# Kernel optimization log

Measured on AMD Instinct MI355X. Metric: run time of the kernel, lower is better.

Reference implementation:

```python
import jax, jax.numpy as jnp
import numpy as np

TABLE_NUM = 16
TABLE_SIZE_LOG2 = 12
T = 1 << TABLE_SIZE_LOG2          # 4096 entries per table
FEAT = 2                          # features per entry (mini_linear in = table_num*2)
Z_DIM = 512
RES_MIN = 16
RES_MAX = 256
IMG = 256
MLP_HIDDEN = 64
OUT_DIM = 3
BATCH = 8
PRIME_Y = np.uint32(2654435761)   # instant-NGP spatial hash prime


def setup_inputs() -> dict:
    key = jax.random.key(0)
    ks = jax.random.split(key, 9)
    d_tab = TABLE_NUM * T * FEAT
    return {
        "z": jax.random.normal(ks[0], (BATCH, Z_DIM), jnp.float32),
        "w_table": jax.random.normal(ks[1], (Z_DIM, d_tab), jnp.float32) * 1e-2,
        "b_table": jnp.zeros((d_tab,), jnp.float32),
        "w1": jax.random.normal(ks[2], (TABLE_NUM * FEAT, MLP_HIDDEN), jnp.float32) * (1.0 / np.sqrt(TABLE_NUM * FEAT)),
        "b1": jnp.zeros((MLP_HIDDEN,), jnp.float32),
        "w2": jax.random.normal(ks[3], (MLP_HIDDEN, MLP_HIDDEN), jnp.float32) * (1.0 / np.sqrt(MLP_HIDDEN)),
        "b2": jnp.zeros((MLP_HIDDEN,), jnp.float32),
        "w3": jax.random.normal(ks[4], (MLP_HIDDEN, OUT_DIM), jnp.float32) * (1.0 / np.sqrt(MLP_HIDDEN)),
        "b3": jnp.zeros((OUT_DIM,), jnp.float32),
    }


def _sample_coords(b):
    c = (jnp.arange(IMG, dtype=jnp.float32) + 0.5) / IMG
    xx, yy = jnp.meshgrid(c, c, indexing="ij")  # torch.meshgrid default
    coords = jnp.stack([xx, yy], axis=-1).reshape(1, -1, 2)
    return jnp.broadcast_to(coords, (b, IMG * IMG, 2))


def _hash_retrieve(tables, coords):
    """tables: B x L x T x F; coords: B x N x 2 in [0,1). Returns B x N x (L*F)."""
    B, L, _, _ = tables.shape
    growth = np.exp((np.log(RES_MAX) - np.log(RES_MIN)) / (L - 1))
    offs = jnp.array([[0, 0], [1, 0], [0, 1], [1, 1]], dtype=jnp.uint32)  # 4 corners
    bidx = jnp.arange(B)[:, None, None]
    feats = []
    for l in range(L):
        res = jnp.float32(RES_MIN * (growth ** l))
        pos = coords * res                      # B,N,2
        pos0 = jnp.floor(pos)
        frac = pos - pos0                       # B,N,2
        corner = pos0.astype(jnp.uint32)[:, :, None, :] + offs[None, None]  # B,N,4,2
        idx = (corner[..., 0] ^ (corner[..., 1] * PRIME_Y)) & jnp.uint32(T - 1)
        f = tables[:, l][bidx, idx.astype(jnp.int32)]        # B,N,4,F gather
        fx, fy = frac[..., 0], frac[..., 1]
        w = jnp.stack([(1 - fx) * (1 - fy), fx * (1 - fy),
                       (1 - fx) * fy,       fx * fy], axis=-1)  # B,N,4
        feats.append(jnp.einsum("bncf,bnc->bnf", f, w))
    return jnp.concatenate(feats, axis=-1)


def reference(z, w_table, b_table, w1, b1, w2, b2, w3, b3):
    B = z.shape[0]
    tables = (z @ w_table + b_table).reshape(B, TABLE_NUM, T, FEAT)
    coords = _sample_coords(B).astype(tables.dtype)
    feat = _hash_retrieve(tables, coords)                    # B,N,L*F
    h = jax.nn.relu(feat @ w1 + b1)
    h = jax.nn.relu(h @ w2 + b2)
    o = jnp.tanh(h @ w3 + b3)                                # B,N,3
    return o.reshape(B, IMG, IMG, OUT_DIM).transpose(0, 3, 1, 2)
```

## Files before the change

kernel.cpp:

```cpp
#include <hip/hip_runtime.h>
#include <cmath>

#define TABLE_NUM 16
#define T_SIZE    4096
#define Z_DIM     512
#define IMG       256
#define D_TAB     (TABLE_NUM * T_SIZE * 2)
#define BATCH     8
#define HID       64
#define N_PIX     (IMG * IMG)
#define PRIME_Y   2654435761u
#define KCHUNK    4
#define KLEN      (Z_DIM / KCHUNK)
#define NG4       (D_TAB / 4)

typedef _Float16 v8h  __attribute__((ext_vector_type(8)));
typedef _Float16 v2h  __attribute__((ext_vector_type(2)));
typedef float    v4f  __attribute__((ext_vector_type(4)));

struct ResArr { float r[TABLE_NUM]; };

__global__ void prep_weights(const float* __restrict__ w1, const float* __restrict__ w2,
                             const float* __restrict__ w3, const float* __restrict__ z,
                             _Float16* __restrict__ w1T, _Float16* __restrict__ w2T,
                             _Float16* __restrict__ w3T, float* __restrict__ zT)
{
    const int t = threadIdx.x;
    for (int i = t; i < HID * 32; i += 256) {
        int n = i >> 5, k = i & 31;
        w1T[i] = (_Float16)w1[k * HID + n];
    }
    for (int i = t; i < HID * HID; i += 256) {
        int n = i >> 6, k = i & 63;
        w2T[i] = (_Float16)w2[k * HID + n];
    }
    for (int i = t; i < 16 * HID; i += 256) {
        int n = i >> 6, k = i & 63;
        w3T[i] = (_Float16)(n < 3 ? w3[k * 3 + n] : 0.f);
    }
    for (int i = t; i < Z_DIM * BATCH; i += 256) {
        int k = i >> 3, b = i & 7;
        zT[i] = z[b * Z_DIM + k];
    }
}

__global__ __launch_bounds__(256) void gen_partial(
    const float* __restrict__ zT, const float* __restrict__ w,
    float* __restrict__ part)
{
    const int c  = blockIdx.x >> 7;
    const int g  = (blockIdx.x & 127) * 256 + threadIdx.x;
    const int k0 = c * KLEN;
    const float4* wp = reinterpret_cast<const float4*>(w) + g;

    float4 acc[BATCH];
#pragma unroll
    for (int b = 0; b < BATCH; ++b) acc[b] = make_float4(0.f, 0.f, 0.f, 0.f);

#pragma unroll 8
    for (int kk = 0; kk < KLEN; ++kk) {
        const int k = k0 + kk;
        float4 wv = wp[(size_t)k * NG4];
        const float* zr = zT + k * BATCH;
#pragma unroll
        for (int b = 0; b < BATCH; ++b) {
            float zv = zr[b];
            acc[b].x = fmaf(zv, wv.x, acc[b].x);
            acc[b].y = fmaf(zv, wv.y, acc[b].y);
            acc[b].z = fmaf(zv, wv.z, acc[b].z);
            acc[b].w = fmaf(zv, wv.w, acc[b].w);
        }
    }

    float4* pp = reinterpret_cast<float4*>(part);
#pragma unroll
    for (int b = 0; b < BATCH; ++b)
        pp[((size_t)(c * BATCH + b) << 15) + g] = acc[b];
}

__global__ __launch_bounds__(256) void gen_reduce(
    const float* __restrict__ part, const float* __restrict__ bt,
    float* __restrict__ tabs)
{
    const int i = blockIdx.x * 256 + threadIdx.x;
    const int b = i >> 15, g = i & (NG4 - 1);
    const float4* pp = reinterpret_cast<const float4*>(part);

    float4 s = pp[((size_t)b << 15) + g];
#pragma unroll
    for (int c = 1; c < KCHUNK; ++c) {
        float4 p = pp[((size_t)(c * BATCH + b) << 15) + g];
        s.x += p.x; s.y += p.y; s.z += p.z; s.w += p.w;
    }
    float4 bv = reinterpret_cast<const float4*>(bt)[g];
    s.x += bv.x; s.y += bv.y; s.z += bv.z; s.w += bv.w;
    reinterpret_cast<float4*>(tabs)[((size_t)b << 15) + g] = s;
}

__global__ __launch_bounds__(256) void hash_mlp(
    const float* __restrict__ tabs,
    const _Float16* __restrict__ w1T, const _Float16* __restrict__ w2T,
    const _Float16* __restrict__ w3T,
    const float* __restrict__ b1, const float* __restrict__ b2,
    const float* __restrict__ b3,
    float* __restrict__ out, ResArr res)
{
    __shared__ _Float16 mbuf[4][64][72];
    const int tid  = threadIdx.x;
    const int wid  = tid >> 6;
    const int lane = tid & 63;
    const int b    = blockIdx.x & 7;
    const int tile = blockIdx.x >> 3;
    const int i0   = (tile >> 4) * 16 + wid * 4;
    const int j0   = (tile & 15) * 16;

    const int di = lane >> 4, dj = lane & 15;
    const float cx = ((float)(i0 + di) + 0.5f) * (1.0f / IMG);
    const float cy = ((float)(j0 + dj) + 0.5f) * (1.0f / IMG);
    const float2* tb2 = reinterpret_cast<const float2*>(tabs + (size_t)b * D_TAB);

#pragma unroll 4
    for (int l = 0; l < TABLE_NUM; ++l) {
        float r  = res.r[l];
        float px = cx * r, py = cy * r;
        float fx0 = floorf(px), fy0 = floorf(py);
        float fx = px - fx0, fy = py - fy0;
        unsigned x0 = (unsigned)(int)fx0, y0 = (unsigned)(int)fy0;
        unsigned hy0 = y0 * PRIME_Y, hy1 = (y0 + 1u) * PRIME_Y;
        unsigned i00 = (x0 ^ hy0) & (T_SIZE - 1);
        unsigned i10 = ((x0 + 1u) ^ hy0) & (T_SIZE - 1);
        unsigned i01 = (x0 ^ hy1) & (T_SIZE - 1);
        unsigned i11 = ((x0 + 1u) ^ hy1) & (T_SIZE - 1);
        const float2* tl = tb2 + l * T_SIZE;
        float2 f00 = tl[i00], f10 = tl[i10], f01 = tl[i01], f11 = tl[i11];
        float w00 = (1.f - fx) * (1.f - fy);
        float w10 = fx * (1.f - fy);
        float w01 = (1.f - fx) * fy;
        float w11 = fx * fy;
        float e0 = f00.x * w00 + f10.x * w10 + f01.x * w01 + f11.x * w11;
        float e1 = f00.y * w00 + f10.y * w10 + f01.y * w01 + f11.y * w11;
        v2h p; p.x = (_Float16)e0; p.y = (_Float16)e1;
        *reinterpret_cast<v2h*>(&mbuf[wid][lane][2 * l]) = p;
    }

    const int arow = lane & 15;
    const int kgrp = lane >> 4;

    float bias1v[4], bias2v[4];
#pragma unroll
    for (int nt = 0; nt < 4; ++nt) {
        bias1v[nt] = b1[nt * 16 + arow];
        bias2v[nt] = b2[nt * 16 + arow];
    }
    const float bias3 = (arow < 3) ? b3[arow] : 0.f;

    v8h a1[4];
#pragma unroll
    for (int mt = 0; mt < 4; ++mt)
        a1[mt] = *reinterpret_cast<const v8h*>(&mbuf[wid][mt * 16 + arow][kgrp * 8]);

    v4f c1[4][4];
#pragma unroll
    for (int nt = 0; nt < 4; ++nt) {
        v8h bf1 = *reinterpret_cast<const v8h*>(&w1T[(nt * 16 + arow) * 32 + kgrp * 8]);
#pragma unroll
        for (int mt = 0; mt < 4; ++mt) {
            v4f c = {0.f, 0.f, 0.f, 0.f};
            c = __builtin_amdgcn_mfma_f32_16x16x32_f16(a1[mt], bf1, c, 0, 0, 0);
#pragma unroll
            for (int e = 0; e < 4; ++e)
                c1[mt][nt][e] = fmaxf(c[e] + bias1v[nt], 0.f);
        }
    }

#pragma unroll
    for (int mt = 0; mt < 4; ++mt)
#pragma unroll
        for (int nt = 0; nt < 4; ++nt)
#pragma unroll
            for (int e = 0; e < 4; ++e)
                mbuf[wid][mt * 16 + kgrp * 4 + e][nt * 16 + arow] = (_Float16)c1[mt][nt][e];

    v8h a2[4][2];
#pragma unroll
    for (int mt = 0; mt < 4; ++mt) {
        a2[mt][0] = *reinterpret_cast<const v8h*>(&mbuf[wid][mt * 16 + arow][kgrp * 8]);
        a2[mt][1] = *reinterpret_cast<const v8h*>(&mbuf[wid][mt * 16 + arow][32 + kgrp * 8]);
    }
    v4f c2[4][4];
#pragma unroll
    for (int nt = 0; nt < 4; ++nt) {
        v8h bf2a = *reinterpret_cast<const v8h*>(&w2T[(nt * 16 + arow) * 64 + kgrp * 8]);
        v8h bf2b = *reinterpret_cast<const v8h*>(&w2T[(nt * 16 + arow) * 64 + 32 + kgrp * 8]);
#pragma unroll
        for (int mt = 0; mt < 4; ++mt) {
            v4f c = {0.f, 0.f, 0.f, 0.f};
            c = __builtin_amdgcn_mfma_f32_16x16x32_f16(a2[mt][0], bf2a, c, 0, 0, 0);
            c = __builtin_amdgcn_mfma_f32_16x16x32_f16(a2[mt][1], bf2b, c, 0, 0, 0);
#pragma unroll
            for (int e = 0; e < 4; ++e)
                c2[mt][nt][e] = fmaxf(c[e] + bias2v[nt], 0.f);
        }
    }

#pragma unroll
    for (int mt = 0; mt < 4; ++mt)
#pragma unroll
        for (int nt = 0; nt < 4; ++nt)
#pragma unroll
            for (int e = 0; e < 4; ++e)
                mbuf[wid][mt * 16 + kgrp * 4 + e][nt * 16 + arow] = (_Float16)c2[mt][nt][e];

#pragma unroll
    for (int mt = 0; mt < 4; ++mt) {
        v8h bf3a = *reinterpret_cast<const v8h*>(&w3T[arow * 64 + kgrp * 8]);
        v8h bf3b = *reinterpret_cast<const v8h*>(&w3T[arow * 64 + 32 + kgrp * 8]);
        v8h a0  = *reinterpret_cast<const v8h*>(&mbuf[wid][mt * 16 + arow][kgrp * 8]);
        v8h a1v = *reinterpret_cast<const v8h*>(&mbuf[wid][mt * 16 + arow][32 + kgrp * 8]);
        v4f c = {0.f, 0.f, 0.f, 0.f};
        c = __builtin_amdgcn_mfma_f32_16x16x32_f16(a0,  bf3a, c, 0, 0, 0);
        c = __builtin_amdgcn_mfma_f32_16x16x32_f16(a1v, bf3b, c, 0, 0, 0);
        if (arow < 3) {
            float4 st;
            st.x = tanhf(c[0] + bias3);
            st.y = tanhf(c[1] + bias3);
            st.z = tanhf(c[2] + bias3);
            st.w = tanhf(c[3] + bias3);
            size_t idx = ((size_t)b * 3 + arow) * N_PIX
                       + (size_t)(i0 + mt) * IMG + j0 + kgrp * 4;
            *reinterpret_cast<float4*>(&out[idx]) = st;
        }
    }
}

extern "C" void kernel_launch(void* const* d_in, const int* in_sizes, int n_in,
                              void* d_out, int out_size, void* d_ws, size_t ws_size,
                              hipStream_t stream)
{
    const float* z  = (const float*)d_in[0];
    const float* wt = (const float*)d_in[1];
    const float* bt = (const float*)d_in[2];
    const float* w1 = (const float*)d_in[3];
    const float* b1 = (const float*)d_in[4];
    const float* w2 = (const float*)d_in[5];
    const float* b2 = (const float*)d_in[6];
    const float* w3 = (const float*)d_in[7];
    const float* b3 = (const float*)d_in[8];
    float* out  = (float*)d_out;

    char* ws = (char*)d_ws;
    float*     tabs = (float*)ws;
    float*     part = (float*)(ws + (4 << 20));
    _Float16*  w1T  = (_Float16*)(ws + (20 << 20));
    _Float16*  w2T  = (_Float16*)(ws + (20 << 20) + 4096);
    _Float16*  w3T  = (_Float16*)(ws + (20 << 20) + 12288);
    float*     zT   = (float*)(ws + (20 << 20) + 16384);

    ResArr ra;
    const double growth = std::exp((std::log(256.0) - std::log(16.0)) / 15.0);
    for (int l = 0; l < TABLE_NUM; ++l)
        ra.r[l] = (float)(16.0 * std::pow(growth, (double)l));

    prep_weights<<<1, 256, 0, stream>>>(w1, w2, w3, z, w1T, w2T, w3T, zT);
    gen_partial<<<KCHUNK * (NG4 / 256), 256, 0, stream>>>(zT, wt, part);
    gen_reduce<<<BATCH * NG4 / 256, 256, 0, stream>>>(part, bt, tabs);
    hash_mlp<<<BATCH * (N_PIX / 256), 256, 0, stream>>>(
        tabs, w1T, w2T, w3T, b1, b2, b3, out, ra);
}
```

Before: 98.40 us.

## Split fused hash+MLP kernel into separate feature and MLP kernels in two batch halves

The fused hash_mlp kernel is split into hash_feat, which gathers and interpolates the hash-grid features and writes fp16 feature vectors to a global workspace buffer, and mlp_eval, which reads those features and runs the MFMA MLP. The work is issued in two passes of four batches each so the feature buffer fits in the reused workspace region. The aim is to let each kernel use fewer registers and schedule better on its own. The cost is a global round-trip of the features plus four launches instead of one.

Measured after the change: 125.5 us. 27.5% more time.

```diff
diff --git a/kernel.cpp b/kernel.cpp
--- a/kernel.cpp
+++ b/kernel.cpp
@@ -97,20 +97,15 @@
     reinterpret_cast<float4*>(tabs)[((size_t)b << 15) + g] = s;
 }
 
-__global__ __launch_bounds__(256) void hash_mlp(
-    const float* __restrict__ tabs,
-    const _Float16* __restrict__ w1T, const _Float16* __restrict__ w2T,
-    const _Float16* __restrict__ w3T,
-    const float* __restrict__ b1, const float* __restrict__ b2,
-    const float* __restrict__ b3,
-    float* __restrict__ out, ResArr res)
-{
-    __shared__ _Float16 mbuf[4][64][72];
+__global__ __launch_bounds__(256) void hash_feat(
+    const float* __restrict__ tabs, _Float16* __restrict__ featbuf,
+    ResArr res, int b0)
+{
     const int tid  = threadIdx.x;
     const int wid  = tid >> 6;
     const int lane = tid & 63;
-    const int b    = blockIdx.x & 7;
-    const int tile = blockIdx.x >> 3;
+    const int b    = b0 + (blockIdx.x & 3);
+    const int tile = blockIdx.x >> 2;
     const int i0   = (tile >> 4) * 16 + wid * 4;
     const int j0   = (tile & 15) * 16;
 
@@ -119,7 +114,8 @@
     const float cy = ((float)(j0 + dj) + 0.5f) * (1.0f / IMG);
     const float2* tb2 = reinterpret_cast<const float2*>(tabs + (size_t)b * D_TAB);
 
-#pragma unroll 4
+    v8h fr[4];
+#pragma unroll
     for (int l = 0; l < TABLE_NUM; ++l) {
         float r  = res.r[l];
         float px = cx * r, py = cy * r;
@@ -139,12 +135,38 @@
         float w11 = fx * fy;
         float e0 = f00.x * w00 + f10.x * w10 + f01.x * w01 + f11.x * w11;
         float e1 = f00.y * w00 + f10.y * w10 + f01.y * w01 + f11.y * w11;
-        v2h p; p.x = (_Float16)e0; p.y = (_Float16)e1;
-        *reinterpret_cast<v2h*>(&mbuf[wid][lane][2 * l]) = p;
-    }
+        fr[l >> 2][(l & 3) * 2]     = (_Float16)e0;
+        fr[l >> 2][(l & 3) * 2 + 1] = (_Float16)e1;
+    }
+
+    _Float16* fp = featbuf + ((size_t)blockIdx.x * 256 + tid) * 32;
+#pragma unroll
+    for (int q = 0; q < 4; ++q)
+        *reinterpret_cast<v8h*>(fp + q * 8) = fr[q];
+}
+
+__global__ __launch_bounds__(256) void mlp_eval(
+    const _Float16* __restrict__ featbuf,
+    const _Float16* __restrict__ w1T, const _Float16* __restrict__ w2T,
+    const _Float16* __restrict__ w3T,
+    const float* __restrict__ b1, const float* __restrict__ b2,
+    const float* __restrict__ b3,
+    float* __restrict__ out, int b0)
+{
+    __shared__ _Float16 mbuf[4][64][72];
+    const int tid  = threadIdx.x;
+    const int wid  = tid >> 6;
+    const int lane = tid & 63;
+    const int b    = b0 + (blockIdx.x & 3);
+    const int tile = blockIdx.x >> 2;
+    const int i0   = (tile >> 4) * 16 + wid * 4;
+    const int j0   = (tile & 15) * 16;
 
     const int arow = lane & 15;
     const int kgrp = lane >> 4;
+
+    const _Float16* fbase = featbuf
+        + ((size_t)blockIdx.x * 4 + wid) * 64 * 32;
 
     float bias1v[4], bias2v[4];
 #pragma unroll
@@ -157,7 +179,7 @@
     v8h a1[4];
 #pragma unroll
     for (int mt = 0; mt < 4; ++mt)
-        a1[mt] = *reinterpret_cast<const v8h*>(&mbuf[wid][mt * 16 + arow][kgrp * 8]);
+        a1[mt] = *reinterpret_cast<const v8h*>(&fbase[(mt * 16 + arow) * 32 + kgrp * 8]);
 
     v4f c1[4][4];
 #pragma unroll
@@ -251,6 +273,7 @@
     char* ws = (char*)d_ws;
     float*     tabs = (float*)ws;
     float*     part = (float*)(ws + (4 << 20));
+    _Float16*  fbuf = (_Float16*)(ws + (4 << 20));
     _Float16*  w1T  = (_Float16*)(ws + (20 << 20));
     _Float16*  w2T  = (_Float16*)(ws + (20 << 20) + 4096);
     _Float16*  w3T  = (_Float16*)(ws + (20 << 20) + 12288);
@@ -264,6 +287,9 @@
     prep_weights<<<1, 256, 0, stream>>>(w1, w2, w3, z, w1T, w2T, w3T, zT);
     gen_partial<<<KCHUNK * (NG4 / 256), 256, 0, stream>>>(zT, wt, part);
     gen_reduce<<<BATCH * NG4 / 256, 256, 0, stream>>>(part, bt, tabs);
-    hash_mlp<<<BATCH * (N_PIX / 256), 256, 0, stream>>>(
-        tabs, w1T, w2T, w3T, b1, b2, b3, out, ra);
-}
+    for (int p = 0; p < 2; ++p) {
+        hash_feat<<<4 * (N_PIX / 256), 256, 0, stream>>>(tabs, fbuf, ra, p * 4);
+        mlp_eval<<<4 * (N_PIX / 256), 256, 0, stream>>>(
+            fbuf, w1T, w2T, w3T, b1, b2, b3, out, p * 4);
+    }
+}
```
